# Optimization experiments

Measured on AMD Instinct MI355X. Metric: run time of the kernel, lower is better.

The kernel has to match this reference:

```python
import jax, jax.numpy as jnp
import numpy as np

BIN_NUM = 256
HIDDEN = 1024
B, S = 128, 1024
FEAT = BIN_NUM - 1          # 255
LAST = FEAT + 3             # 258, used as d_k in the original code


def setup_inputs() -> dict:
    key = jax.random.key(0)
    ks = jax.random.split(key, 8)

    def lin(k, out_d, in_d):
        # kaiming_uniform_ with relu nonlinearity: bound = sqrt(6/in_d)
        bound = np.sqrt(6.0 / in_d)
        return jax.random.uniform(k, (out_d, in_d), jnp.float32, -bound, bound)

    return {
        "input_tensor": jax.random.normal(ks[0], (B, S, LAST), jnp.float32),
        "kW": lin(ks[1], HIDDEN, FEAT), "kb": jnp.zeros((HIDDEN,), jnp.float32),
        "vW": lin(ks[2], HIDDEN, FEAT), "vb": jnp.zeros((HIDDEN,), jnp.float32),
        "qW": lin(ks[3], HIDDEN, 3),    "qb": jnp.zeros((HIDDEN,), jnp.float32),
        "W1": lin(ks[4], HIDDEN // 2, HIDDEN),      "b1": jnp.zeros((HIDDEN // 2,), jnp.float32),
        "W2": lin(ks[5], HIDDEN // 4, HIDDEN // 2), "b2": jnp.zeros((HIDDEN // 4,), jnp.float32),
        "W3": lin(ks[6], 2, HIDDEN // 4),           "b3": jnp.zeros((2,), jnp.float32),
    }


def reference(input_tensor, kW, kb, vW, vb, qW, qb, W1, b1, W2, b2, W3, b3):
    d_k = input_tensor.shape[-1]                      # NOTE: full last dim (258)
    feats = input_tensor[..., :FEAT]                  # [B,S,255]
    archi = input_tensor[:, 0, FEAT:][:, None, :]     # [B,1,3]

    k = jnp.einsum('bsf,hf->bsh', feats, kW) + kb     # [B,S,H]
    v = jnp.einsum('bsf,hf->bsh', feats, vW) + vb     # [B,S,H]
    q = jnp.einsum('bqf,hf->bqh', archi, qW) + qb     # [B,1,H]

    scores = jnp.einsum('bqh,bsh->bqs', q, k) / jnp.sqrt(jnp.float32(d_k))
    attn = jax.nn.softmax(scores, axis=-1)            # [B,1,S]
    res = jnp.einsum('bqs,bsh->bqh', attn, v)[:, 0, :]  # squeeze -> [B,H]

    # classifier (dropout is identity at inference)
    h = jax.nn.relu(res @ W1.T + b1)
    h = jax.nn.relu(h @ W2.T + b2)
    return h @ W3.T + b3                              # [B,2]
```

## Files before the change

### kernel.cpp

```cpp
#include <hip/hip_runtime.h>
#include <stdint.h>

#define NBATCH 128
#define SEQ    1024
#define ROWE   258
#define NPART  8

#define WS_KQP   0
#define WS_PART  524288
#define WS_WF    2654208
#define WS_REST  2785280
#define WS_H1P   3309568


static __device__ __forceinline__ float fexp2(float x){ return __builtin_amdgcn_exp2f(x); }

typedef float floatx4 __attribute__((ext_vector_type(4)));
static __device__ __forceinline__ floatx4 load16a8(const float* p) {
    floatx4 r;
    __builtin_memcpy(&r, __builtin_assume_aligned(p, 8), 16);
    return r;
}

__global__ __launch_bounds__(256) void qk_kernel(const float* __restrict__ in,
    const float* __restrict__ kW, const float* __restrict__ qW,
    const float* __restrict__ qb, float* __restrict__ kqp,
    float* __restrict__ h1pre, float* __restrict__ out)
{
    __shared__ float qv[2][256];
    const int bb = blockIdx.x;
    const int hh = blockIdx.y;
    const int t  = threadIdx.x;
    const int b0 = bb * 2;
    if (hh == 0) {
        h1pre[(size_t)b0 * 512 + t]             = 0.f;
        h1pre[(size_t)b0 * 512 + 256 + t]       = 0.f;
        h1pre[(size_t)(b0 + 1) * 512 + t]       = 0.f;
        h1pre[(size_t)(b0 + 1) * 512 + 256 + t] = 0.f;
        if (t < 4) out[b0 * 2 + t] = 0.f;
    }
    const int h = hh * 256 + t;
    const float w0 = qW[h * 3 + 0], w1 = qW[h * 3 + 1], w2 = qW[h * 3 + 2], bq = qb[h];
    #pragma unroll
    for (int u = 0; u < 2; u++) {
        const size_t abase = (size_t)(b0 + u) * (SEQ * ROWE) + 255;
        qv[u][t] = bq + in[abase] * w0 + in[abase + 1] * w1 + in[abase + 2] * w2;
    }
    __syncthreads();
    const int col = (t < 255) ? t : 254;
    const float* kWp = kW + (size_t)(hh * 256) * 255 + col;
    float acc0 = 0.f, acc1 = 0.f;
    #pragma unroll 16
    for (int i = 0; i < 256; i++) {
        const float kv = kWp[(size_t)i * 255];
        acc0 = fmaf(qv[0][i], kv, acc0);
        acc1 = fmaf(qv[1][i], kv, acc1);
    }
    kqp[(size_t)((hh << 7) + b0) * 256 + t]       = (t < 255) ? acc0 : 0.f;
    kqp[(size_t)((hh << 7) + b0 + 1) * 256 + t]   = (t < 255) ? acc1 : 0.f;
}

__global__ __launch_bounds__(256, 6) void attn_kernel(const float* __restrict__ in,
                                                      const float* __restrict__ kqp,
                                                      float* __restrict__ part)
{
    __shared__ float sM[4], sL[4], sacc[4][256];
    const int p = blockIdx.x, b = blockIdx.y;
    const int t = threadIdx.x, w = t >> 6, lane = t & 63;

    const float SCALE = (float)(1.4426950408889634 / 16.062378404209142);
    float k[4];
    {
        float s0=0.f, s1=0.f, s2=0.f, s3=0.f;
        #pragma unroll
        for (int hh = 0; hh < 4; hh++) {
            const float4 u = *(const float4*)(kqp + (size_t)((hh << 7) + b) * 256 + lane * 4);
            s0 += u.x; s1 += u.y; s2 += u.z; s3 += u.w;
        }
        k[0] = s0 * SCALE; k[1] = s1 * SCALE; k[2] = s2 * SCALE; k[3] = s3 * SCALE;
    }

    const float* rp = in + ((size_t)b * SEQ + p * 128 + w * 32) * ROWE + lane * 4;

    float x[4], xn[4], a[4] = {0.f, 0.f, 0.f, 0.f};
    {
        const floatx4 v = load16a8(rp);
        x[0] = v.x; x[1] = v.y; x[2] = v.z; x[3] = v.w;
    }
    rp += ROWE;
    float m = -INFINITY, l = 0.f;

    #pragma unroll 8
    for (int i = 0; i < 32; i++) {
        if (i < 31) {
            const floatx4 v = load16a8(rp);
            xn[0] = v.x; xn[1] = v.y; xn[2] = v.z; xn[3] = v.w;
            rp += ROWE;
        }
        float d = fmaf(x[0], k[0], fmaf(x[1], k[1], fmaf(x[2], k[2], x[3] * k[3])));
        #pragma unroll
        for (int off = 32; off > 0; off >>= 1) d += __shfl_xor(d, off, 64);
        const float mn = fmaxf(m, d);
        const float cc = fexp2(m - mn);
        const float wt = fexp2(d - mn);
        l = fmaf(l, cc, wt);
        #pragma unroll
        for (int j = 0; j < 4; j++) a[j] = fmaf(a[j], cc, wt * x[j]);
        m = mn;
        if (i < 31) {
            #pragma unroll
            for (int j = 0; j < 4; j++) x[j] = xn[j];
        }
    }

    #pragma unroll
    for (int j = 0; j < 4; j += 2)
        *(float2*)(&sacc[w][lane * 4 + j]) = make_float2(a[j], a[j+1]);
    if (lane == 0) { sM[w] = m; sL[w] = l; }
    __syncthreads();

    const float M  = fmaxf(fmaxf(sM[0], sM[1]), fmaxf(sM[2], sM[3]));
    const float c0 = fexp2(sM[0] - M), c1 = fexp2(sM[1] - M);
    const float c2 = fexp2(sM[2] - M), c3 = fexp2(sM[3] - M);
    const float acc = c0 * sacc[0][t] + c1 * sacc[1][t] + c2 * sacc[2][t] + c3 * sacc[3][t];
    float* o = part + ((size_t)b * NPART + p) * 260;
    o[t] = acc;
    if (t == 0) {
        o[256] = M;
        o[257] = c0 * sL[0] + c1 * sL[1] + c2 * sL[2] + c3 * sL[3];
    }
}

__global__ __launch_bounds__(256) void comb_kernel(const float* __restrict__ part,
                                                   float* __restrict__ wf)
{
    const int b = blockIdx.x, t = threadIdx.x;
    const float* pb = part + (size_t)b * NPART * 260;
    float M = -INFINITY;
    #pragma unroll
    for (int p = 0; p < NPART; p++) M = fmaxf(M, pb[p * 260 + 256]);
    float L = 0.f, acc = 0.f;
    #pragma unroll
    for (int p = 0; p < NPART; p++) {
        const float cc = fexp2(pb[p * 260 + 256] - M);
        L   = fmaf(cc, pb[p * 260 + 257], L);
        acc = fmaf(cc, pb[p * 260 + t], acc);
    }
    wf[b * 256 + t] = (t < 255) ? acc / L : 0.f;
}

__global__ __launch_bounds__(512) void res_kernel(const float* __restrict__ vW,
                                                  const float* __restrict__ vb,
                                                  const float* __restrict__ wf,
                                                  float* __restrict__ resT)
{
    __shared__ float vws[8][256];
    __shared__ float wfs[64][130];
    const int g = blockIdx.x, t = threadIdx.x;
    #pragma unroll
    for (int i = 0; i < 4; i++) {
        const int idx = i * 512 + t, f = idx & 255, hh = idx >> 8;
        vws[hh][f] = (f < 255) ? vW[(g * 8 + hh) * 255 + f] : 0.f;
    }
    const int b = t & 127, ho = t >> 7;
    const int fl = t & 63, wv = t >> 6;
    float acc0 = 0.f, acc1 = 0.f;
    for (int c = 0; c < 4; c++) {
        __syncthreads();
        #pragma unroll
        for (int i = 0; i < 16; i++) {
            const int bb = i * 8 + wv;
            wfs[fl][bb] = wf[bb * 256 + c * 64 + fl];
        }
        __syncthreads();
        #pragma unroll 8
        for (int f = 0; f < 64; f++) {
            const float w2 = wfs[f][b];
            acc0 = fmaf(w2, vws[ho][c * 64 + f], acc0);
            acc1 = fmaf(w2, vws[ho + 4][c * 64 + f], acc1);
        }
    }
    const int h0 = g * 8 + ho, h1 = h0 + 4;
    resT[h0 * 128 + b] = acc0 + vb[h0];
    resT[h1 * 128 + b] = acc1 + vb[h1];
}

__global__ __launch_bounds__(256) void h1_kernel(const float* __restrict__ W1,
                                                 const float* __restrict__ resT,
                                                 float* __restrict__ h1pre)
{
    __shared__ float W1s[16][256];
    __shared__ float ress[64][66];
    const int j0 = blockIdx.x * 16, b0 = blockIdx.y * 64, h0 = blockIdx.z * 256;
    const int t = threadIdx.x;
    #pragma unroll
    for (int i = 0; i < 16; i++) {
        const int idx = i * 256 + t, hl = idx & 255, jj = idx >> 8;
        W1s[jj][hl] = W1[(j0 + jj) * 1024 + h0 + hl];
    }
    const int bb = t & 63, jg = t >> 6;
    float acc[4] = {0.f, 0.f, 0.f, 0.f};
    for (int sc = 0; sc < 4; sc++) {
        __syncthreads();
        {
            const int bl = t & 63, wvv = t >> 6;
            #pragma unroll
            for (int i = 0; i < 16; i++) {
                const int hl = i * 4 + wvv;
                ress[hl][bl] = resT[(h0 + sc * 64 + hl) * 128 + b0 + bl];
            }
        }
        __syncthreads();
        #pragma unroll 4
        for (int hl = 0; hl < 64; hl++) {
            const float rv = ress[hl][bb];
            acc[0] = fmaf(rv, W1s[jg * 4 + 0][sc * 64 + hl], acc[0]);
            acc[1] = fmaf(rv, W1s[jg * 4 + 1][sc * 64 + hl], acc[1]);
            acc[2] = fmaf(rv, W1s[jg * 4 + 2][sc * 64 + hl], acc[2]);
            acc[3] = fmaf(rv, W1s[jg * 4 + 3][sc * 64 + hl], acc[3]);
        }
    }
    #pragma unroll
    for (int k = 0; k < 4; k++)
        atomicAdd(&h1pre[(size_t)(b0 + bb) * 512 + j0 + jg * 4 + k], acc[k]);
}

__global__ __launch_bounds__(256) void h2out_kernel(const float* __restrict__ W2,
    const float* __restrict__ b1, const float* __restrict__ b2,
    const float* __restrict__ W3, const float* __restrict__ b3,
    const float* __restrict__ h1pre, float* __restrict__ out)
{
    __shared__ float W2s[8][512];
    __shared__ float h1s[64][66];
    __shared__ float po[4][64][2];
    const int j20 = blockIdx.x * 8, b0 = blockIdx.y * 64;
    const int t = threadIdx.x;
    #pragma unroll
    for (int i = 0; i < 16; i++) {
        const int idx = i * 256 + t, jl = idx & 511, jj = idx >> 9;
        W2s[jj][jl] = W2[(j20 + jj) * 512 + jl];
    }
    const int bb = t & 63, jg = t >> 6;
    float acc[2] = {0.f, 0.f};
    for (int sc = 0; sc < 8; sc++) {
        __syncthreads();
        {
            const int jl = t & 63, wvv = t >> 6;
            #pragma unroll
            for (int i = 0; i < 16; i++) {
                const int bl = i * 4 + wvv;
                const float v = h1pre[(size_t)(b0 + bl) * 512 + sc * 64 + jl] + b1[sc * 64 + jl];
                h1s[jl][bl] = fmaxf(v, 0.f);
            }
        }
        __syncthreads();
        #pragma unroll 4
        for (int jl = 0; jl < 64; jl++) {
            const float hv = h1s[jl][bb];
            acc[0] = fmaf(hv, W2s[jg * 2 + 0][sc * 64 + jl], acc[0]);
            acc[1] = fmaf(hv, W2s[jg * 2 + 1][sc * 64 + jl], acc[1]);
        }
    }
    float p0 = 0.f, p1 = 0.f;
    #pragma unroll
    for (int k = 0; k < 2; k++) {
        const int j2 = j20 + jg * 2 + k;
        const float h2v = fmaxf(acc[k] + b2[j2], 0.f);
        p0 = fmaf(h2v, W3[j2],       p0);
        p1 = fmaf(h2v, W3[256 + j2], p1);
    }
    po[jg][bb][0] = p0;
    po[jg][bb][1] = p1;
    __syncthreads();
    if (t < 128) {
        const int b = t & 63, o = t >> 6;
        float s = po[0][b][o] + po[1][b][o] + po[2][b][o] + po[3][b][o];
        if (blockIdx.x == 0) s += b3[o];
        atomicAdd(&out[(b0 + b) * 2 + o], s);
    }
}

extern "C" void kernel_launch(void* const* d_in, const int* in_sizes, int n_in,
                              void* d_out, int out_size, void* d_ws, size_t ws_size,
                              hipStream_t stream)
{
    (void)in_sizes; (void)n_in; (void)out_size; (void)ws_size;
    const float* in = (const float*)d_in[0];
    const float* kW = (const float*)d_in[1];
    const float* vW = (const float*)d_in[3];
    const float* vb = (const float*)d_in[4];
    const float* qW = (const float*)d_in[5];
    const float* qb = (const float*)d_in[6];
    const float* W1 = (const float*)d_in[7];
    const float* b1 = (const float*)d_in[8];
    const float* W2 = (const float*)d_in[9];
    const float* b2 = (const float*)d_in[10];
    const float* W3 = (const float*)d_in[11];
    const float* b3 = (const float*)d_in[12];

    char* ws = (char*)d_ws;
    float* kqp   = (float*)(ws + WS_KQP);
    float* part  = (float*)(ws + WS_PART);
    float* wf    = (float*)(ws + WS_WF);
    float* resT  = (float*)(ws + WS_REST);
    float* h1pre = (float*)(ws + WS_H1P);

    qk_kernel   <<<dim3(64, 4),         256, 0, stream>>>(in, kW, qW, qb, kqp, h1pre, (float*)d_out);
    attn_kernel <<<dim3(NPART, NBATCH), 256, 0, stream>>>(in, kqp, part);
    comb_kernel <<<128,                 256, 0, stream>>>(part, wf);
    res_kernel  <<<128,                 512, 0, stream>>>(vW, vb, wf, resT);
    h1_kernel   <<<dim3(32, 2, 4),      256, 0, stream>>>(W1, resT, h1pre);
    h2out_kernel<<<dim3(32, 2),         256, 0, stream>>>(W2, b1, b2, W3, b3, h1pre, (float*)d_out);
}
```

Baseline: 284.1 us.

## Fuse softmax combine and classifier MLP into a single per-batch tail kernel

Replaces the combine, value-projection, and two classifier GEMM kernels with one kernel in which each block handles two batch rows end to end, keeping intermediates in shared memory. This removes three launches, the intermediate global buffers, the atomics and the zero-initialisation. In exchange, every block re-reads the full vW, W1 and W2 weight matrices with per-thread row walks (vW is uncoalesced), and only 64 blocks run, so the tail may become bandwidth- or latency-bound.

```diff
diff --git a/kernel.cpp b/kernel.cpp
--- a/kernel.cpp
+++ b/kernel.cpp
@@ -8,9 +8,6 @@
 
 #define WS_KQP   0
 #define WS_PART  524288
-#define WS_WF    2654208
-#define WS_REST  2785280
-#define WS_H1P   3309568
 
 
 static __device__ __forceinline__ float fexp2(float x){ return __builtin_amdgcn_exp2f(x); }
@@ -24,21 +21,13 @@
 
 __global__ __launch_bounds__(256) void qk_kernel(const float* __restrict__ in,
     const float* __restrict__ kW, const float* __restrict__ qW,
-    const float* __restrict__ qb, float* __restrict__ kqp,
-    float* __restrict__ h1pre, float* __restrict__ out)
+    const float* __restrict__ qb, float* __restrict__ kqp)
 {
     __shared__ float qv[2][256];
     const int bb = blockIdx.x;
     const int hh = blockIdx.y;
     const int t  = threadIdx.x;
     const int b0 = bb * 2;
-    if (hh == 0) {
-        h1pre[(size_t)b0 * 512 + t]             = 0.f;
-        h1pre[(size_t)b0 * 512 + 256 + t]       = 0.f;
-        h1pre[(size_t)(b0 + 1) * 512 + t]       = 0.f;
-        h1pre[(size_t)(b0 + 1) * 512 + 256 + t] = 0.f;
-        if (t < 4) out[b0 * 2 + t] = 0.f;
-    }
     const int h = hh * 256 + t;
     const float w0 = qW[h * 3 + 0], w1 = qW[h * 3 + 1], w2 = qW[h * 3 + 2], bq = qb[h];
     #pragma unroll
@@ -131,152 +120,98 @@
     }
 }
 
-__global__ __launch_bounds__(256) void comb_kernel(const float* __restrict__ part,
-                                                   float* __restrict__ wf)
-{
-    const int b = blockIdx.x, t = threadIdx.x;
-    const float* pb = part + (size_t)b * NPART * 260;
-    float M = -INFINITY;
+__global__ __launch_bounds__(512) void tail_kernel(const float* __restrict__ part,
+    const float* __restrict__ vW, const float* __restrict__ vb,
+    const float* __restrict__ W1, const float* __restrict__ b1,
+    const float* __restrict__ W2, const float* __restrict__ b2,
+    const float* __restrict__ W3, const float* __restrict__ b3,
+    float* __restrict__ out)
+{
+    __shared__ float wfs[2][256];
+    __shared__ float resv[2][1024];
+    __shared__ float h1v[2][512];
+    __shared__ float h2v[2][256];
+    const int g = blockIdx.x, t = threadIdx.x;
+    const int b0 = g * 2;
+
+    {
+        const int bl = t >> 8, f = t & 255;
+        const float* pb = part + (size_t)(b0 + bl) * NPART * 260;
+        float M = -INFINITY;
+        #pragma unroll
+        for (int p = 0; p < NPART; p++) M = fmaxf(M, pb[p * 260 + 256]);
+        float L = 0.f, acc = 0.f;
+        #pragma unroll
+        for (int p = 0; p < NPART; p++) {
+            const float cc = fexp2(pb[p * 260 + 256] - M);
+            L   = fmaf(cc, pb[p * 260 + 257], L);
+            acc = fmaf(cc, pb[p * 260 + f], acc);
+        }
+        wfs[bl][f] = (f < 255) ? acc / L : 0.f;
+    }
+    __syncthreads();
+
     #pragma unroll
-    for (int p = 0; p < NPART; p++) M = fmaxf(M, pb[p * 260 + 256]);
-    float L = 0.f, acc = 0.f;
-    #pragma unroll
-    for (int p = 0; p < NPART; p++) {
-        const float cc = fexp2(pb[p * 260 + 256] - M);
-        L   = fmaf(cc, pb[p * 260 + 257], L);
-        acc = fmaf(cc, pb[p * 260 + t], acc);
-    }
-    wf[b * 256 + t] = (t < 255) ? acc / L : 0.f;
-}
-
-__global__ __launch_bounds__(512) void res_kernel(const float* __restrict__ vW,
-                                                  const float* __restrict__ vb,
-                                                  const float* __restrict__ wf,
-                                                  float* __restrict__ resT)
-{
-    __shared__ float vws[8][256];
-    __shared__ float wfs[64][130];
-    const int g = blockIdx.x, t = threadIdx.x;
-    #pragma unroll
-    for (int i = 0; i < 4; i++) {
-        const int idx = i * 512 + t, f = idx & 255, hh = idx >> 8;
-        vws[hh][f] = (f < 255) ? vW[(g * 8 + hh) * 255 + f] : 0.f;
-    }
-    const int b = t & 127, ho = t >> 7;
-    const int fl = t & 63, wv = t >> 6;
-    float acc0 = 0.f, acc1 = 0.f;
-    for (int c = 0; c < 4; c++) {
-        __syncthreads();
-        #pragma unroll
-        for (int i = 0; i < 16; i++) {
-            const int bb = i * 8 + wv;
-            wfs[fl][bb] = wf[bb * 256 + c * 64 + fl];
-        }
-        __syncthreads();
+    for (int r = 0; r < 2; r++) {
+        const int h = t + r * 512;
+        const float* vr = vW + (size_t)h * 255;
+        float a0 = 0.f, a1 = 0.f;
+        #pragma unroll 5
+        for (int f = 0; f < 255; f++) {
+            const float v = vr[f];
+            a0 = fmaf(v, wfs[0][f], a0);
+            a1 = fmaf(v, wfs[1][f], a1);
+        }
+        resv[0][h] = a0 + vb[h];
+        resv[1][h] = a1 + vb[h];
+    }
+    __syncthreads();
+
+    {
+        const float* wr = W1 + (size_t)t * 1024;
+        float a0 = 0.f, a1 = 0.f;
         #pragma unroll 8
-        for (int f = 0; f < 64; f++) {
-            const float w2 = wfs[f][b];
-            acc0 = fmaf(w2, vws[ho][c * 64 + f], acc0);
-            acc1 = fmaf(w2, vws[ho + 4][c * 64 + f], acc1);
-        }
-    }
-    const int h0 = g * 8 + ho, h1 = h0 + 4;
-    resT[h0 * 128 + b] = acc0 + vb[h0];
-    resT[h1 * 128 + b] = acc1 + vb[h1];
-}
-
-__global__ __launch_bounds__(256) void h1_kernel(const float* __restrict__ W1,
-                                                 const float* __restrict__ resT,
-                                                 float* __restrict__ h1pre)
-{
-    __shared__ float W1s[16][256];
-    __shared__ float ress[64][66];
-    const int j0 = blockIdx.x * 16, b0 = blockIdx.y * 64, h0 = blockIdx.z * 256;
-    const int t = threadIdx.x;
-    #pragma unroll
-    for (int i = 0; i < 16; i++) {
-        const int idx = i * 256 + t, hl = idx & 255, jj = idx >> 8;
-        W1s[jj][hl] = W1[(j0 + jj) * 1024 + h0 + hl];
-    }
-    const int bb = t & 63, jg = t >> 6;
-    float acc[4] = {0.f, 0.f, 0.f, 0.f};
-    for (int sc = 0; sc < 4; sc++) {
-        __syncthreads();
-        {
-            const int bl = t & 63, wvv = t >> 6;
+        for (int h = 0; h < 1024; h += 4) {
+            const float4 w4 = *(const float4*)(wr + h);
+            a0 = fmaf(w4.x, resv[0][h],   fmaf(w4.y, resv[0][h+1],
+                 fmaf(w4.z, resv[0][h+2], fmaf(w4.w, resv[0][h+3], a0))));
+            a1 = fmaf(w4.x, resv[1][h],   fmaf(w4.y, resv[1][h+1],
+                 fmaf(w4.z, resv[1][h+2], fmaf(w4.w, resv[1][h+3], a1))));
+        }
+        h1v[0][t] = fmaxf(a0 + b1[t], 0.f);
+        h1v[1][t] = fmaxf(a1 + b1[t], 0.f);
+    }
+    __syncthreads();
+
+    {
+        const int bl = t >> 8, j2 = t & 255;
+        const float* wr = W2 + (size_t)j2 * 512;
+        float a = 0.f;
+        #pragma unroll 8
+        for (int j = 0; j < 512; j += 4) {
+            const float4 w4 = *(const float4*)(wr + j);
+            a = fmaf(w4.x, h1v[bl][j],   fmaf(w4.y, h1v[bl][j+1],
+                fmaf(w4.z, h1v[bl][j+2], fmaf(w4.w, h1v[bl][j+3], a))));
+        }
+        h2v[bl][j2] = fmaxf(a + b2[j2], 0.f);
+    }
+    __syncthreads();
+
+    {
+        const int w = t >> 6, lane = t & 63;
+        if (w < 4) {
+            const int bl = w >> 1, o = w & 1;
+            const float* wr = W3 + o * 256;
+            float a = 0.f;
             #pragma unroll
-            for (int i = 0; i < 16; i++) {
-                const int hl = i * 4 + wvv;
-                ress[hl][bl] = resT[(h0 + sc * 64 + hl) * 128 + b0 + bl];
+            for (int j = 0; j < 4; j++) {
+                const int j2 = lane + j * 64;
+                a = fmaf(wr[j2], h2v[bl][j2], a);
             }
-        }
-        __syncthreads();
-        #pragma unroll 4
-        for (int hl = 0; hl < 64; hl++) {
-            const float rv = ress[hl][bb];
-            acc[0] = fmaf(rv, W1s[jg * 4 + 0][sc * 64 + hl], acc[0]);
-            acc[1] = fmaf(rv, W1s[jg * 4 + 1][sc * 64 + hl], acc[1]);
-            acc[2] = fmaf(rv, W1s[jg * 4 + 2][sc * 64 + hl], acc[2]);
-            acc[3] = fmaf(rv, W1s[jg * 4 + 3][sc * 64 + hl], acc[3]);
-        }
-    }
-    #pragma unroll
-    for (int k = 0; k < 4; k++)
-        atomicAdd(&h1pre[(size_t)(b0 + bb) * 512 + j0 + jg * 4 + k], acc[k]);
-}
-
-__global__ __launch_bounds__(256) void h2out_kernel(const float* __restrict__ W2,
-    const float* __restrict__ b1, const float* __restrict__ b2,
-    const float* __restrict__ W3, const float* __restrict__ b3,
-    const float* __restrict__ h1pre, float* __restrict__ out)
-{
-    __shared__ float W2s[8][512];
-    __shared__ float h1s[64][66];
-    __shared__ float po[4][64][2];
-    const int j20 = blockIdx.x * 8, b0 = blockIdx.y * 64;
-    const int t = threadIdx.x;
-    #pragma unroll
-    for (int i = 0; i < 16; i++) {
-        const int idx = i * 256 + t, jl = idx & 511, jj = idx >> 9;
-        W2s[jj][jl] = W2[(j20 + jj) * 512 + jl];
-    }
-    const int bb = t & 63, jg = t >> 6;
-    float acc[2] = {0.f, 0.f};
-    for (int sc = 0; sc < 8; sc++) {
-        __syncthreads();
-        {
-            const int jl = t & 63, wvv = t >> 6;
             #pragma unroll
-            for (int i = 0; i < 16; i++) {
-                const int bl = i * 4 + wvv;
-                const float v = h1pre[(size_t)(b0 + bl) * 512 + sc * 64 + jl] + b1[sc * 64 + jl];
-                h1s[jl][bl] = fmaxf(v, 0.f);
-            }
-        }
-        __syncthreads();
-        #pragma unroll 4
-        for (int jl = 0; jl < 64; jl++) {
-            const float hv = h1s[jl][bb];
-            acc[0] = fmaf(hv, W2s[jg * 2 + 0][sc * 64 + jl], acc[0]);
-            acc[1] = fmaf(hv, W2s[jg * 2 + 1][sc * 64 + jl], acc[1]);
-        }
-    }
-    float p0 = 0.f, p1 = 0.f;
-    #pragma unroll
-    for (int k = 0; k < 2; k++) {
-        const int j2 = j20 + jg * 2 + k;
-        const float h2v = fmaxf(acc[k] + b2[j2], 0.f);
-        p0 = fmaf(h2v, W3[j2],       p0);
-        p1 = fmaf(h2v, W3[256 + j2], p1);
-    }
-    po[jg][bb][0] = p0;
-    po[jg][bb][1] = p1;
-    __syncthreads();
-    if (t < 128) {
-        const int b = t & 63, o = t >> 6;
-        float s = po[0][b][o] + po[1][b][o] + po[2][b][o] + po[3][b][o];
-        if (blockIdx.x == 0) s += b3[o];
-        atomicAdd(&out[(b0 + b) * 2 + o], s);
+            for (int off = 32; off > 0; off >>= 1) a += __shfl_xor(a, off, 64);
+            if (lane == 0) out[(b0 + bl) * 2 + o] = a + b3[o];
+        }
     }
 }
 
@@ -299,16 +234,11 @@
     const float* b3 = (const float*)d_in[12];
 
     char* ws = (char*)d_ws;
-    float* kqp   = (float*)(ws + WS_KQP);
-    float* part  = (float*)(ws + WS_PART);
-    float* wf    = (float*)(ws + WS_WF);
-    float* resT  = (float*)(ws + WS_REST);
-    float* h1pre = (float*)(ws + WS_H1P);
-
-    qk_kernel   <<<dim3(64, 4),         256, 0, stream>>>(in, kW, qW, qb, kqp, h1pre, (float*)d_out);
+    float* kqp  = (float*)(ws + WS_KQP);
+    float* part = (float*)(ws + WS_PART);
+
+    qk_kernel   <<<dim3(64, 4),         256, 0, stream>>>(in, kW, qW, qb, kqp);
     attn_kernel <<<dim3(NPART, NBATCH), 256, 0, stream>>>(in, kqp, part);
-    comb_kernel <<<128,                 256, 0, stream>>>(part, wf);
-    res_kernel  <<<128,                 512, 0, stream>>>(vW, vb, wf, resT);
-    h1_kernel   <<<dim3(32, 2, 4),      256, 0, stream>>>(W1, resT, h1pre);
-    h2out_kernel<<<dim3(32, 2),         256, 0, stream>>>(W2, b1, b2, W3, b3, h1pre, (float*)d_out);
-}
+    tail_kernel <<<64,                  512, 0, stream>>>(part, vW, vb, W1, b1,
+                                                          W2, b2, W3, b3, (float*)d_out);
+}
```

Measured after the change: 409.1 us. 1.44x slower.
